# Kernel optimization log

Hardware: AMD Instinct MI355X
Metric: run time of the kernel (lower is better)

The kernel has to match this reference:

```python
import jax, jax.numpy as jnp
import numpy as np

B, T, D, H = 2, 2048, 1024, 16
HD = D // H            # head dim = 64
WINDOW = 512           # sliding-window size
EPS = 1e-6
ROPE_BASE = 10000.0


def setup_inputs() -> dict:
    key = jax.random.key(0)
    ks = jax.random.split(key, 5)
    s = 0.02  # init scale for dense kernels
    return {
        "x": jax.random.normal(ks[0], (B, T, D), jnp.float32),
        "Wq": jax.random.normal(ks[1], (D, D), jnp.float32) * s,
        "Wk": jax.random.normal(ks[2], (D, D), jnp.float32) * s,
        "Wv": jax.random.normal(ks[3], (D, D), jnp.float32) * s,
        "Wo": jax.random.normal(ks[4], (D, D), jnp.float32) * s,
        "q_scale": jnp.ones((HD,), jnp.float32),
        "k_scale": jnp.ones((HD,), jnp.float32),
        "sink_logit": jnp.zeros((H,), jnp.float32),
    }


def _rmsnorm(x, scale):
    # x: [..., HD]
    var = jnp.mean(jnp.square(x), axis=-1, keepdims=True)
    return x * jax.lax.rsqrt(var + EPS) * scale


def _rope(x):
    # x: [B, H, T, HD]; standard rotate-half RoPE over the full head dim
    half = HD // 2
    inv_freq = 1.0 / (ROPE_BASE ** (jnp.arange(0, HD, 2, dtype=jnp.float32) / HD))  # [half]
    t = jnp.arange(T, dtype=jnp.float32)
    freqs = t[:, None] * inv_freq[None, :]                # [T, half]
    emb = jnp.concatenate([freqs, freqs], axis=-1)        # [T, HD]
    cos = jnp.cos(emb)[None, None]                        # [1,1,T,HD]
    sin = jnp.sin(emb)[None, None]
    x1, x2 = x[..., :half], x[..., half:]
    rot = jnp.concatenate([-x2, x1], axis=-1)
    return x * cos + rot * sin


def reference(x, Wq, Wk, Wv, Wo, q_scale, k_scale, sink_logit):
    # projections -> [B, T, H, HD]
    q = (x @ Wq).reshape(B, T, H, HD)
    k = (x @ Wk).reshape(B, T, H, HD)
    v = (x @ Wv).reshape(B, T, H, HD)
    # QK RMSNorm over head dim
    q = _rmsnorm(q, q_scale)
    k = _rmsnorm(k, k_scale)
    # -> [B, H, T, HD], then RoPE
    q = _rope(q.transpose(0, 2, 1, 3))
    k = _rope(k.transpose(0, 2, 1, 3))
    v = v.transpose(0, 2, 1, 3)
    # causal sliding-window mask
    idx = jnp.arange(T)
    rel = idx[None, :] - idx[:, None]                     # key - query
    mask = ((rel <= 0) & (rel > -WINDOW))[None, None]     # [1,1,T,T]
    scale = HD ** (-0.5)
    scores = jnp.einsum('bhtd,bhsd->bhts', q, k) * scale
    scores = jnp.where(mask, scores, -jnp.inf)
    # sink-augmented softmax: append per-head sink logit to denominator
    sink = jnp.broadcast_to(sink_logit.reshape(1, H, 1, 1), (B, H, T, 1))
    aug = jnp.concatenate([scores.astype(jnp.float32), sink.astype(jnp.float32)], axis=-1)
    weights = jax.nn.softmax(aug, axis=-1)[..., :T].astype(scores.dtype)
    out = jnp.einsum('bhts,bhsd->bhtd', weights, v)
    out = out.transpose(0, 2, 1, 3).reshape(B, T, D)
    return out @ Wo
```

## Files before the change

kernel.cpp:

```cpp
#include <hip/hip_runtime.h>
#include <math.h>

#define CB 2
#define CT 2048
#define CD 1024
#define CH 16
#define CHD 64
#define CWINDOW 512

typedef __bf16 bf16x8 __attribute__((ext_vector_type(8)));
typedef float floatx4 __attribute__((ext_vector_type(4)));

__device__ __forceinline__ unsigned short f2bf(float f) {
  union { float f; unsigned int u; } v;
  v.f = f;
  unsigned int u = v.u;
  u += 0x7fffu + ((u >> 16) & 1u);
  return (unsigned short)(u >> 16);
}
__device__ __forceinline__ unsigned short f2bf_trunc(float f) {
  union { float f; unsigned int u; } v;
  v.f = f;
  return (unsigned short)(v.u >> 16);
}
__device__ __forceinline__ float bf2f(unsigned int h) {
  union { unsigned int u; float f; } v;
  v.u = h << 16;
  return v.f;
}

__global__ __launch_bounds__(256) void cvt_all(const float* __restrict__ x,
                                               const float* __restrict__ Wq,
                                               const float* __restrict__ Wk,
                                               const float* __restrict__ Wv,
                                               const float* __restrict__ Wo,
                                               unsigned short* __restrict__ xb,
                                               unsigned short* __restrict__ WqT,
                                               unsigned short* __restrict__ WkT,
                                               unsigned short* __restrict__ WvT,
                                               unsigned short* __restrict__ WoT) {
  const int z = blockIdx.z;
  if (z < 4) {
    const float* W = z == 0 ? Wq : z == 1 ? Wk : z == 2 ? Wv : Wo;
    unsigned short* Wt = z == 0 ? WqT : z == 1 ? WkT : z == 2 ? WvT : WoT;
    __shared__ float tile[64][65];
    const int k0 = blockIdx.x * 64, n0 = blockIdx.y * 64;
    const int c = threadIdx.x & 63, r4 = threadIdx.x >> 6;
#pragma unroll
    for (int i = 0; i < 16; ++i) {
      int r = i * 4 + r4;
      tile[r][c] = W[(size_t)(k0 + r) * CD + n0 + c];
    }
    __syncthreads();
#pragma unroll
    for (int i = 0; i < 16; ++i) {
      int r = i * 4 + r4;
      Wt[(size_t)(n0 + r) * CD + k0 + c] = f2bf(tile[c][r]);
    }
  } else {
    const int idx = (z - 4) * 256 + blockIdx.y * 16 + blockIdx.x;
    const int i = idx * 256 + threadIdx.x;
    float4 a = ((const float4*)x)[i * 2];
    float4 b = ((const float4*)x)[i * 2 + 1];
    uint4 o;
    o.x = (unsigned int)f2bf(a.x) | ((unsigned int)f2bf(a.y) << 16);
    o.y = (unsigned int)f2bf(a.z) | ((unsigned int)f2bf(a.w) << 16);
    o.z = (unsigned int)f2bf(b.x) | ((unsigned int)f2bf(b.y) << 16);
    o.w = (unsigned int)f2bf(b.z) | ((unsigned int)f2bf(b.w) << 16);
    ((uint4*)xb)[i] = o;
  }
}

__device__ __forceinline__ void async16(const unsigned short* g, unsigned short* l) {
  __builtin_amdgcn_global_load_lds(
      (const __attribute__((address_space(1))) unsigned int*)g,
      (__attribute__((address_space(3))) unsigned int*)l, 16, 0, 0);
}

__device__ __forceinline__ bf16x8 frag64(const unsigned short* base, int row, int ks, int lane) {
  const int phys = (((ks << 2) + (lane >> 4)) ^ (lane & 7)) << 3;
  return *(const bf16x8*)&base[(row << 6) + phys];
}

template <int MODE, int BM>
__device__ __forceinline__ void mfma_gemm_body(const unsigned short* __restrict__ A,
                                               const unsigned short* __restrict__ Bt,
                                               void* __restrict__ Cout,
                                               const float* __restrict__ scale,
                                               float oscale, int m0, int n0,
                                               unsigned short* __restrict__ As,
                                               unsigned short* __restrict__ Bs) {
  constexpr int K = CD;
  constexpr int MT = BM / 32;
  const int tid = threadIdx.x;
  const int wave = tid >> 6, lane = tid & 63;
  const int mq = (wave & 1) * (BM / 2), nq = (wave >> 1) * 64;

  floatx4 acc[MT][4] = {};
  const int l7 = lane & 7, l8 = lane >> 3;
  const int sxc = (l7 ^ l8) * 8;
  const int fr = lane & 15;

  for (int k0 = 0; k0 < K; k0 += 64) {
    __syncthreads();
#pragma unroll
    for (int it = 0; it < BM / 32; ++it) {
      const int s = wave * (BM / 32) + it;
      async16(A + (size_t)(m0 + s * 8 + l8) * K + k0 + sxc, &As[s * 512]);
    }
#pragma unroll
    for (int it = 0; it < 4; ++it) {
      const int s = wave * 4 + it;
      async16(Bt + (size_t)(n0 + s * 8 + l8) * K + k0 + sxc, &Bs[s * 512]);
    }
    __syncthreads();
#pragma unroll
    for (int ks = 0; ks < 2; ++ks) {
      bf16x8 af[MT], bg[4];
#pragma unroll
      for (int mt = 0; mt < MT; ++mt)
        af[mt] = frag64(As, mq + mt * 16 + fr, ks, lane);
#pragma unroll
      for (int nt = 0; nt < 4; ++nt)
        bg[nt] = frag64(Bs, nq + nt * 16 + fr, ks, lane);
#pragma unroll
      for (int mt = 0; mt < MT; ++mt)
#pragma unroll
        for (int nt = 0; nt < 4; ++nt)
          acc[mt][nt] = __builtin_amdgcn_mfma_f32_16x16x32_bf16(af[mt], bg[nt], acc[mt][nt], 0, 0, 0);
    }
  }

  if (MODE == 1) {
    const int c = lane & 15;
    const int g = lane >> 4;
    const int hh = (n0 + nq) >> 6;
    const float kf = -0.2878231366242557f;
    const float inv0 = __expf((float)c * kf);
    const float inv1 = __expf((float)(16 + c) * kf);
    float sc[4];
#pragma unroll
    for (int nt = 0; nt < 4; ++nt) sc[nt] = scale[nt * 16 + c];
#pragma unroll
    for (int mt = 0; mt < MT; ++mt) {
#pragma unroll
      for (int i = 0; i < 4; ++i) {
        const int m = m0 + mq + mt * 16 + g * 4 + i;
        const int b = m >> 11, t = m & (CT - 1);
        float v0 = acc[mt][0][i], v1 = acc[mt][1][i];
        float v2 = acc[mt][2][i], v3 = acc[mt][3][i];
        float ss = v0 * v0 + v1 * v1 + v2 * v2 + v3 * v3;
#pragma unroll
        for (int off = 8; off > 0; off >>= 1) ss += __shfl_xor(ss, off);
        const float rs = rsqrtf(ss * (1.0f / 64.0f) + 1e-6f);
        v0 *= rs * sc[0];
        v1 *= rs * sc[1];
        v2 *= rs * sc[2];
        v3 *= rs * sc[3];
        const float tf = (float)t;
        const float a0 = tf * inv0, a1 = tf * inv1;
        const float s0 = __sinf(a0), c0 = __cosf(a0);
        const float s1 = __sinf(a1), c1 = __cosf(a1);
        unsigned short* dst = (unsigned short*)Cout + ((size_t)(b * CH + hh) * CT + t) * CHD;
        ushort4 o;
        o.x = f2bf((v0 * c0 - v2 * s0) * oscale);
        o.y = f2bf((v1 * c1 - v3 * s1) * oscale);
        o.z = f2bf((v2 * c0 + v0 * s0) * oscale);
        o.w = f2bf((v3 * c1 + v1 * s1) * oscale);
        *(ushort4*)&dst[4 * c] = o;
      }
    }
  } else {
#pragma unroll
    for (int mt = 0; mt < MT; ++mt) {
#pragma unroll
      for (int nt = 0; nt < 4; ++nt) {
        const int col = n0 + nq + nt * 16 + (lane & 15);
        if (MODE == 2) {
          const int mb = m0 + mq + mt * 16 + (lane >> 4) * 4;
          const int b = mb >> 11, t = mb & (CT - 1);
          const int h = col >> 6, d = col & 63;
          ushort4 o;
          o.x = f2bf(acc[mt][nt][0]);
          o.y = f2bf(acc[mt][nt][1]);
          o.z = f2bf(acc[mt][nt][2]);
          o.w = f2bf(acc[mt][nt][3]);
          *(ushort4*)&((unsigned short*)Cout)[((size_t)(b * CH + h) * CHD + d) * CT + t] = o;
        } else {
#pragma unroll
          for (int i = 0; i < 4; ++i) {
            const int m = m0 + mq + mt * 16 + (lane >> 4) * 4 + i;
            ((float*)Cout)[(size_t)m * CD + col] = acc[mt][nt][i];
          }
        }
      }
    }
  }
}

__global__ __launch_bounds__(256, 3) void gemm_qkv_mfma(const unsigned short* __restrict__ xb,
                                                        const unsigned short* __restrict__ WqT,
                                                        const unsigned short* __restrict__ WkT,
                                                        const unsigned short* __restrict__ WvT,
                                                        unsigned short* __restrict__ Qh,
                                                        unsigned short* __restrict__ Kh,
                                                        unsigned short* __restrict__ Vt,
                                                        const float* __restrict__ q_scale,
                                                        const float* __restrict__ k_scale) {
  __shared__ unsigned short As[128 * 64];
  __shared__ unsigned short Bs[128 * 64];
  const unsigned int L = blockIdx.x + 32u * blockIdx.y + 256u * blockIdx.z;
  const int m0 = (int)((L >> 3) & 31u) * 128;
  const int n0 = (int)(L & 7u) * 128;
  const int bz = (int)(L >> 8);
  if (bz == 2) {
    mfma_gemm_body<2, 128>(xb, WvT, Vt, nullptr, 1.0f, m0, n0, As, Bs);
  } else if (bz == 0) {
    mfma_gemm_body<1, 128>(xb, WqT, Qh, q_scale, 0.125f, m0, n0, As, Bs);
  } else {
    mfma_gemm_body<1, 128>(xb, WkT, Kh, k_scale, 1.0f, m0, n0, As, Bs);
  }
}

__global__ __launch_bounds__(256, 3) void gemm_out_mfma(const unsigned short* __restrict__ AO,
                                                        const unsigned short* __restrict__ WoT,
                                                        float* __restrict__ out) {
  __shared__ unsigned short As[64 * 64];
  __shared__ unsigned short Bs[128 * 64];
  const unsigned int L = blockIdx.x + 64u * blockIdx.y;
  const int m0 = (int)(L >> 3) * 64;
  const int n0 = (int)(L & 7u) * 128;
  mfma_gemm_body<0, 64>(AO, WoT, out, nullptr, 1.0f, m0, n0, As, Bs);
}

__global__ __launch_bounds__(256, 2) void attn_mfma(const unsigned short* __restrict__ Qh,
                                                    const unsigned short* __restrict__ Kh,
                                                    const unsigned short* __restrict__ Vt,
                                                    const float* __restrict__ sink_logit,
                                                    unsigned short* __restrict__ AO) {
  __shared__ unsigned short Qs[128 * 64];
  __shared__ unsigned short Ks[2][64 * 64];
  __shared__ unsigned short Vs[2][64 * 64];
  __shared__ unsigned short Ps[128 * 72];

  const int tid = threadIdx.x;
  const int w = tid >> 6, lane = tid & 63;
  const unsigned int L = blockIdx.x + 16u * blockIdx.y;
  const int qb = (int)((L >> 3) & 15u);
  const int bh = (int)(L & 7u) * 4 + (int)(L >> 7);
  const int b = bh >> 4, h = bh & 15;
  const int q0 = qb * 128;
  const unsigned short* Qb = Qh + (size_t)bh * CT * CHD;
  const unsigned short* Kb = Kh + (size_t)bh * CT * CHD;
  const unsigned short* Vb = Vt + (size_t)bh * CHD * CT;

  const int l7 = lane & 7, l8 = lane >> 3;
  const int sx8 = (l7 ^ l8) * 8;

  const int kb_lo = (qb >= 4) ? (qb * 2 - 8) : 0;
  const int kb_hi = qb * 2 + 1;

#pragma unroll
  for (int s = 0; s < 4; ++s) {
    const int slab = w * 4 + s;
    async16(Qb + (size_t)(q0 + slab * 8 + l8) * CHD + sx8, &Qs[slab * 512]);
  }
#pragma unroll
  for (int s = 0; s < 2; ++s) {
    const int slab = w * 2 + s;
    const int row = slab * 8 + l8;
    async16(Kb + (size_t)(kb_lo * 64 + row) * CHD + sx8, &Ks[0][slab * 512]);
    async16(Vb + (size_t)row * CT + kb_lo * 64 + sx8, &Vs[0][slab * 512]);
  }
  __syncthreads();

  bf16x8 qf[2][2];
#pragma unroll
  for (int nt = 0; nt < 2; ++nt)
#pragma unroll
    for (int ks = 0; ks < 2; ++ks)
      qf[nt][ks] = frag64(Qs, w * 32 + nt * 16 + (lane & 15), ks, lane);

  floatx4 acc[4][2] = {};
  float lsum[2] = {0.f, 0.f};
  const int qw = q0 + w * 32;

  int cur = 0;
  for (int kb = kb_lo; kb <= kb_hi; ++kb) {
    if (kb < kb_hi) {
#pragma unroll
      for (int s = 0; s < 2; ++s) {
        const int slab = w * 2 + s;
        const int row = slab * 8 + l8;
        async16(Kb + (size_t)((kb + 1) * 64 + row) * CHD + sx8, &Ks[cur ^ 1][slab * 512]);
        async16(Vb + (size_t)row * CT + (kb + 1) * 64 + sx8, &Vs[cur ^ 1][slab * 512]);
      }
    }

    const int kmin = kb * 64, kmax = kb * 64 + 63;
    if (!(kmin > qw + 31 || kmax <= qw - CWINDOW)) {
      const unsigned short* Kc = Ks[cur];
      const unsigned short* Vc = Vs[cur];

      floatx4 st[4][2] = {};
#pragma unroll
      for (int ks = 0; ks < 2; ++ks) {
        bf16x8 kf[4];
#pragma unroll
        for (int mt = 0; mt < 4; ++mt)
          kf[mt] = frag64(Kc, mt * 16 + (lane & 15), ks, lane);
        __builtin_amdgcn_s_setprio(1);
#pragma unroll
        for (int mt = 0; mt < 4; ++mt)
#pragma unroll
          for (int nt = 0; nt < 2; ++nt)
            st[mt][nt] = __builtin_amdgcn_mfma_f32_16x16x32_bf16(kf[mt], qf[nt][ks], st[mt][nt], 0, 0, 0);
        __builtin_amdgcn_s_setprio(0);
      }

      const bool need_c = (kmax > qw);
      const bool need_w = (kmin <= qw + 31 - CWINDOW);
#pragma unroll
      for (int mt = 0; mt < 4; ++mt) {
#pragma unroll
        for (int nt = 0; nt < 2; ++nt) {
          const int s_base = kb * 64 + mt * 16 + (lane >> 4) * 4;
          const int t_g = q0 + w * 32 + nt * 16 + (lane & 15);
          ushort4 pk;
          float psum = 0.f;
#pragma unroll
          for (int i = 0; i < 4; ++i) {
            float sv = st[mt][nt][i];
            if (need_c || need_w) {
              const int s_g = s_base + i;
              const bool ok = (!need_c || (s_g <= t_g)) && (!need_w || (s_g > t_g - CWINDOW));
              sv = ok ? sv : -INFINITY;
            }
            const unsigned short pb = f2bf_trunc(__expf(sv));
            ((unsigned short*)&pk)[i] = pb;
            psum += bf2f(pb);
          }
          lsum[nt] += psum;
          const int qrow = w * 32 + nt * 16 + (lane & 15);
          const int scol = mt * 16 + (lane >> 4) * 4;
          *(ushort4*)&Ps[qrow * 72 + scol] = pk;
        }
      }

#pragma unroll
      for (int ks = 0; ks < 2; ++ks) {
        bf16x8 vf[4], pf[2];
#pragma unroll
        for (int mt = 0; mt < 4; ++mt)
          vf[mt] = frag64(Vc, mt * 16 + (lane & 15), ks, lane);
#pragma unroll
        for (int nt = 0; nt < 2; ++nt) {
          const int qrow = w * 32 + nt * 16 + (lane & 15);
          pf[nt] = *(const bf16x8*)&Ps[qrow * 72 + ks * 32 + (lane >> 4) * 8];
        }
        __builtin_amdgcn_s_setprio(1);
#pragma unroll
        for (int mt = 0; mt < 4; ++mt)
#pragma unroll
          for (int nt = 0; nt < 2; ++nt)
            acc[mt][nt] = __builtin_amdgcn_mfma_f32_16x16x32_bf16(vf[mt], pf[nt], acc[mt][nt], 0, 0, 0);
        __builtin_amdgcn_s_setprio(0);
      }
    }

    asm volatile("s_waitcnt vmcnt(0)" ::: "memory");
    __builtin_amdgcn_s_barrier();
    cur ^= 1;
  }

  const float sinkw = __expf(sink_logit[h]);
  float inv[2];
#pragma unroll
  for (int nt = 0; nt < 2; ++nt) {
    float l = lsum[nt];
    l += __shfl_xor(l, 16);
    l += __shfl_xor(l, 32);
    inv[nt] = 1.0f / (l + sinkw);
  }
#pragma unroll
  for (int mt = 0; mt < 4; ++mt) {
#pragma unroll
    for (int nt = 0; nt < 2; ++nt) {
      const int t_g = q0 + w * 32 + nt * 16 + (lane & 15);
      const int d0 = mt * 16 + (lane >> 4) * 4;
      ushort4 o;
      o.x = f2bf(acc[mt][nt][0] * inv[nt]);
      o.y = f2bf(acc[mt][nt][1] * inv[nt]);
      o.z = f2bf(acc[mt][nt][2] * inv[nt]);
      o.w = f2bf(acc[mt][nt][3] * inv[nt]);
      *(ushort4*)&AO[(size_t)(b * CT + t_g) * CD + h * CHD + d0] = o;
    }
  }
}

extern "C" void kernel_launch(void* const* d_in, const int* in_sizes, int n_in,
                              void* d_out, int out_size, void* d_ws, size_t ws_size,
                              hipStream_t stream) {
  (void)in_sizes;
  (void)n_in;
  (void)out_size;
  (void)ws_size;
  const float* x = (const float*)d_in[0];
  const float* Wq = (const float*)d_in[1];
  const float* Wk = (const float*)d_in[2];
  const float* Wv = (const float*)d_in[3];
  const float* Wo = (const float*)d_in[4];
  const float* q_scale = (const float*)d_in[5];
  const float* k_scale = (const float*)d_in[6];
  const float* sink = (const float*)d_in[7];
  float* out = (float*)d_out;

  const size_t per = (size_t)CB * CH * CT * CHD;
  unsigned short* Qh = (unsigned short*)d_ws;
  unsigned short* Kh = Qh + per;
  unsigned short* Vt = Kh + per;
  unsigned short* AO = Vt + per;
  unsigned short* xb = AO + per;
  unsigned short* WqT = xb + per;
  unsigned short* WkT = WqT + (size_t)CD * CD;
  unsigned short* WvT = WkT + (size_t)CD * CD;
  unsigned short* WoT = WvT + (size_t)CD * CD;

  dim3 blk(256);
  cvt_all<<<dim3(16, 16, 12), blk, 0, stream>>>(x, Wq, Wk, Wv, Wo, xb, WqT, WkT, WvT, WoT);
  gemm_qkv_mfma<<<dim3(32, 8, 3), blk, 0, stream>>>(xb, WqT, WkT, WvT, Qh, Kh, Vt, q_scale, k_scale);
  attn_mfma<<<dim3(CT / 128, CB * CH), blk, 0, stream>>>(Qh, Kh, Vt, sink, AO);
  gemm_out_mfma<<<dim3(64, 8), blk, 0, stream>>>(AO, WoT, out);
}
```

Baseline: 156.5 us.

## Compute softmax row sums via MFMA with ones and remap GEMM block order for L2 reuse

Result: no change. 156.6 us (+0.1%).

```diff
diff --git a/kernel.cpp b/kernel.cpp
--- a/kernel.cpp
+++ b/kernel.cpp
@@ -210,9 +210,16 @@
   __shared__ unsigned short As[128 * 64];
   __shared__ unsigned short Bs[128 * 64];
   const unsigned int L = blockIdx.x + 32u * blockIdx.y + 256u * blockIdx.z;
-  const int m0 = (int)((L >> 3) & 31u) * 128;
-  const int n0 = (int)(L & 7u) * 128;
-  const int bz = (int)(L >> 8);
+  const unsigned int x = L & 7u;
+  const unsigned int j = L >> 3;
+  const unsigned int gm = x & 3u;
+  const unsigned int gw = x >> 2;
+  const unsigned int jm = j & 7u;
+  const unsigned int jp = j >> 3;
+  const int m0 = (int)(gm * 8u + jm) * 128;
+  const unsigned int vp = gw * 12u + jp;
+  const int n0 = (int)(vp & 7u) * 128;
+  const int bz = (int)(vp >> 3);
   if (bz == 2) {
     mfma_gemm_body<2, 128>(xb, WvT, Vt, nullptr, 1.0f, m0, n0, As, Bs);
   } else if (bz == 0) {
@@ -228,8 +235,12 @@
   __shared__ unsigned short As[64 * 64];
   __shared__ unsigned short Bs[128 * 64];
   const unsigned int L = blockIdx.x + 64u * blockIdx.y;
-  const int m0 = (int)(L >> 3) * 64;
-  const int n0 = (int)(L & 7u) * 128;
+  const unsigned int x = L & 7u;
+  const unsigned int j = L >> 3;
+  const unsigned int jm = j & 7u;
+  const unsigned int jp = j >> 3;
+  const int m0 = (int)(x * 8u + jm) * 64;
+  const int n0 = (int)jp * 128;
   mfma_gemm_body<0, 64>(AO, WoT, out, nullptr, 1.0f, m0, n0, As, Bs);
 }
 
@@ -281,8 +292,12 @@
     for (int ks = 0; ks < 2; ++ks)
       qf[nt][ks] = frag64(Qs, w * 32 + nt * 16 + (lane & 15), ks, lane);
 
+  bf16x8 vones;
+#pragma unroll
+  for (int i = 0; i < 8; ++i) vones[i] = (__bf16)1.0f;
+
   floatx4 acc[4][2] = {};
-  float lsum[2] = {0.f, 0.f};
+  floatx4 lsacc[2] = {};
   const int qw = q0 + w * 32;
 
   int cur = 0;
@@ -327,7 +342,6 @@
           const int s_base = kb * 64 + mt * 16 + (lane >> 4) * 4;
           const int t_g = q0 + w * 32 + nt * 16 + (lane & 15);
           ushort4 pk;
-          float psum = 0.f;
 #pragma unroll
           for (int i = 0; i < 4; ++i) {
             float sv = st[mt][nt][i];
@@ -336,11 +350,8 @@
               const bool ok = (!need_c || (s_g <= t_g)) && (!need_w || (s_g > t_g - CWINDOW));
               sv = ok ? sv : -INFINITY;
             }
-            const unsigned short pb = f2bf_trunc(__expf(sv));
-            ((unsigned short*)&pk)[i] = pb;
-            psum += bf2f(pb);
+            ((unsigned short*)&pk)[i] = f2bf_trunc(__expf(sv));
           }
-          lsum[nt] += psum;
           const int qrow = w * 32 + nt * 16 + (lane & 15);
           const int scol = mt * 16 + (lane >> 4) * 4;
           *(ushort4*)&Ps[qrow * 72 + scol] = pk;
@@ -364,6 +375,9 @@
 #pragma unroll
           for (int nt = 0; nt < 2; ++nt)
             acc[mt][nt] = __builtin_amdgcn_mfma_f32_16x16x32_bf16(vf[mt], pf[nt], acc[mt][nt], 0, 0, 0);
+#pragma unroll
+        for (int nt = 0; nt < 2; ++nt)
+          lsacc[nt] = __builtin_amdgcn_mfma_f32_16x16x32_bf16(vones, pf[nt], lsacc[nt], 0, 0, 0);
         __builtin_amdgcn_s_setprio(0);
       }
     }
@@ -376,12 +390,7 @@
   const float sinkw = __expf(sink_logit[h]);
   float inv[2];
 #pragma unroll
-  for (int nt = 0; nt < 2; ++nt) {
-    float l = lsum[nt];
-    l += __shfl_xor(l, 16);
-    l += __shfl_xor(l, 32);
-    inv[nt] = 1.0f / (l + sinkw);
-  }
+  for (int nt = 0; nt < 2; ++nt) inv[nt] = 1.0f / (lsacc[nt][0] + sinkw);
 #pragma unroll
   for (int mt = 0; mt < 4; ++mt) {
 #pragma unroll
```
